# Kernel tuning notes

Hardware: AMD Instinct MI355X
Metric: run time of the kernel (lower is better)

## Reference

```python
import jax, jax.numpy as jnp
import numpy as np

A = -0.75  # torch bicubic coefficient
SCALES = [1.0, 0.9, 0.8, 0.7, 0.6]  # level=5
SOFTMAX_SCALE = 10.0
RES_SCALE = 1.0
ESCAPE_NAN = 1e-4


def _cubic_w(d):
    d = jnp.abs(d)
    return jnp.where(d <= 1.0, ((A + 2.0) * d - (A + 3.0)) * d * d + 1.0,
                     jnp.where(d < 2.0, ((A * d - 5.0 * A) * d + 8.0 * A) * d - 4.0 * A, 0.0))


def _resize_axis(x, out_size, axis):
    # bicubic, align_corners=True, 4-tap cubic conv with border clamp (matches torch)
    in_size = x.shape[axis]
    src = jnp.arange(out_size, dtype=jnp.float32) * (float(in_size - 1) / float(out_size - 1))
    i0 = jnp.floor(src).astype(jnp.int32)
    frac = src - i0.astype(jnp.float32)
    idx = jnp.clip(jnp.stack([i0 - 1, i0, i0 + 1, i0 + 2], 0), 0, in_size - 1)  # [4,out]
    w = jnp.stack([_cubic_w(frac + 1.0), _cubic_w(frac), _cubic_w(1.0 - frac), _cubic_w(2.0 - frac)], 0)  # [4,out]
    xm = jnp.moveaxis(x, axis, 0)
    g = xm[idx]  # [4,out,...]
    out = jnp.einsum('ko...,ko->o...', g, w)
    return jnp.moveaxis(out, 0, axis)


def bicubic_resize(x, oh, ow):
    return _resize_axis(_resize_axis(x, oh, 2), ow, 3)


def prelu(x, a):
    return jnp.where(x >= 0, x, a * x)


def conv1x1(x, W, b):
    # x [B,C,H,W], W [O,C], b [O]
    return jnp.einsum('oc,bchw->bohw', W, x) + b[None, :, None, None]


def extract_patches(x):
    # x [B,C,H,W] -> [B, H*W, C, 3, 3], 'same' padding, stride 1 (torch unfold order C,kh,kw)
    B, C, H, Wd = x.shape
    xp = jnp.pad(x, ((0, 0), (0, 0), (1, 1), (1, 1)))
    sl = [xp[:, :, dy:dy + H, dx:dx + Wd] for dy in range(3) for dx in range(3)]
    p = jnp.stack(sl, 0).reshape(3, 3, B, C, H, Wd)
    p = jnp.transpose(p, (2, 4, 5, 3, 0, 1))  # [B,H,W,C,3,3]
    return p.reshape(B, H * Wd, C, 3, 3)


def setup_inputs() -> dict:
    key = jax.random.key(0)
    ks = jax.random.split(key, 8)
    B, C, H, Wd = 2, 64, 64, 64
    Cm = 32
    return {
        'input': jax.random.normal(ks[0], (B, C, H, Wd), jnp.float32),
        'input_ref': jax.random.normal(ks[1], (B, C, H, Wd), jnp.float32),
        'Wb': jax.random.normal(ks[2], (Cm, C), jnp.float32) * 0.1,
        'bb': jax.random.normal(ks[3], (Cm,), jnp.float32) * 0.01,
        'Wm': jax.random.normal(ks[4], (Cm, C), jnp.float32) * 0.1,
        'bm': jax.random.normal(ks[5], (Cm,), jnp.float32) * 0.01,
        'Wa': jax.random.normal(ks[6], (C, C), jnp.float32) * 0.1,
        'ba': jax.random.normal(ks[7], (C,), jnp.float32) * 0.01,
        'a_prelu': jnp.full((1,), 0.25, jnp.float32),
    }


def reference(input, input_ref, Wb, bb, Wm, bm, Wa, ba, a_prelu):
    B, C, H, Wd = input.shape
    a = a_prelu[0]
    match_base = prelu(conv1x1(input, Wb, bb), a)  # [B,Cm,H,W]

    w_list, rw_list = [], []
    for s in SCALES:
        ref = input_ref if s == 1.0 else bicubic_resize(input_ref, int(H * s), int(Wd * s))
        base = prelu(conv1x1(ref, Wa, ba), a)   # conv_assembly
        rw_list.append(extract_patches(base))   # [B,Li,C,3,3]
        m = prelu(conv1x1(ref, Wm, bm), a)      # conv_match
        w_list.append(extract_patches(m))       # [B,Li,Cm,3,3]
    w = jnp.concatenate(w_list, axis=1)    # [B,L,Cm,3,3]
    rw = jnp.concatenate(rw_list, axis=1)  # [B,L,C,3,3]

    dn = ('NCHW', 'OIHW', 'NCHW')

    def per_sample(xi, wi, rwi):
        # xi [Cm,H,W]; wi [L,Cm,3,3]; rwi [L,C,3,3]
        nrm = jnp.maximum(jnp.sqrt(jnp.sum(wi * wi, axis=(1, 2, 3), keepdims=True)), ESCAPE_NAN)
        wn = wi / nrm
        scores = jax.lax.conv_general_dilated(xi[None], wn, (1, 1), [(1, 1), (1, 1)], dimension_numbers=dn)[0]  # [L,H,W]
        yi = jax.nn.softmax(scores * SOFTMAX_SCALE, axis=0)
        # conv_transpose2d(yi, rwi, stride=1, padding=1) == conv2d with flipped, transposed kernel, pad 1
        k = jnp.transpose(rwi, (1, 0, 2, 3))[:, :, ::-1, ::-1]  # [C,L,3,3]
        out = jax.lax.conv_general_dilated(yi[None], k, (1, 1), [(1, 1), (1, 1)], dimension_numbers=dn)[0] / 4.0
        return out  # [C,H,W]

    y = jax.vmap(per_sample)(match_base, w, rw)
    return y + input * RES_SCALE
```

## Files before the change

### kernel.cpp

```cpp
#include <hip/hip_runtime.h>
#include <stdint.h>


typedef __attribute__((ext_vector_type(8))) short bf16x8;
typedef __attribute__((ext_vector_type(4))) float f32x4;
typedef unsigned short ushort_t;

#define L_TOT  13326
#define NCHT   417
#define NPIX   4096
#define BCHUNK_E 9216
#define RCHUNK_E 18432
#define LOG2E10 14.4269504f
#define CT 256

__device__ __forceinline__ float cubw(float d) {
  d = fabsf(d);
  if (d <= 1.f) return (1.25f * d - 2.25f) * d * d + 1.f;
  if (d < 2.f)  return ((-0.75f * d + 3.75f) * d - 6.f) * d + 3.f;
  return 0.f;
}

__device__ __forceinline__ void decode_l(int l, int& S, int& off) {
  if (l < 4096)       { S = 64; off = 0; }
  else if (l < 7345)  { S = 57; off = 4096; }
  else if (l < 9946)  { S = 51; off = 7345; }
  else if (l < 11882) { S = 44; off = 9946; }
  else                { S = 38; off = 11882; }
}

__device__ __forceinline__ ushort_t f2bf(float f) {
  union { float f; uint32_t u; } v; v.f = f;
  uint32_t r = (v.u + 0x7fffu + ((v.u >> 16) & 1u)) >> 16;
  return (ushort_t)r;
}

__device__ __forceinline__ float preluf(float x, float a) { return x >= 0.f ? x : a * x; }

__device__ __forceinline__ void gll16(const ushort_t* g, ushort_t* l) {
  __builtin_amdgcn_global_load_lds(
      (const __attribute__((address_space(1))) unsigned int*)g,
      (__attribute__((address_space(3))) unsigned int*)l, 16, 0, 0);
}

__global__ void k_convref(const float* __restrict__ inref,
                          const float* __restrict__ Wm, const float* __restrict__ bm,
                          const float* __restrict__ Wa, const float* __restrict__ ba,
                          const float* __restrict__ ap,
                          float* __restrict__ mref, float* __restrict__ aref) {
  __shared__ float T[64][CT];
  __shared__ float Wy[CT][5], Wx[CT][5];
  __shared__ int   IY[CT], IX[CT];
  int blk = blockIdx.x;
  int oh = blk & 1; int lt = (blk >> 1) % 53; int b = blk / 106;
  int l0 = lt * CT;
  int tid = threadIdx.x;
  float a = ap[0];
  {
    int gl = l0 + tid;
    if (gl < L_TOT) {
      int S, off; decode_l(gl, S, off);
      int li = gl - off; int ly = li / S, lx = li % S;
      if (S == 64) {
        IY[tid] = -1; IX[tid] = ly * 64 + lx;
      } else {
        float sc = (float)(63.0 / (double)(S - 1));
        float sy = (float)ly * sc, sx = (float)lx * sc;
        int iy = (int)floorf(sy), ix = (int)floorf(sx);
        float fy = sy - (float)iy, fx = sx - (float)ix;
        IY[tid] = iy; IX[tid] = ix;
        Wy[tid][0] = cubw(fy + 1.f); Wy[tid][1] = cubw(fy);
        Wy[tid][2] = cubw(1.f - fy); Wy[tid][3] = cubw(2.f - fy);
        Wx[tid][0] = cubw(fx + 1.f); Wx[tid][1] = cubw(fx);
        Wx[tid][2] = cubw(1.f - fx); Wx[tid][3] = cubw(2.f - fx);
      }
    }
  }
  __syncthreads();
  for (int i = tid; i < 64 * CT; i += 256) {
    int c = i >> 8; int l2 = i & 255;
    int gl = l0 + l2;
    float val = 0.f;
    if (gl < L_TOT) {
      const float* img = inref + (size_t)(b * 64 + c) * 4096;
      int iy = IY[l2];
      if (iy == -1) {
        val = img[IX[l2]];
      } else {
        int ix = IX[l2];
        #pragma unroll
        for (int t = 0; t < 4; ++t) {
          int ty = iy - 1 + t; ty = ty < 0 ? 0 : (ty > 63 ? 63 : ty);
          float rv = 0.f;
          #pragma unroll
          for (int u = 0; u < 4; ++u) {
            int tx = ix - 1 + u; tx = tx < 0 ? 0 : (tx > 63 ? 63 : tx);
            rv += Wx[l2][u] * img[ty * 64 + tx];
          }
          val += Wy[l2][t] * rv;
        }
      }
    }
    T[c][l2] = val;
  }
  __syncthreads();
  int gl = l0 + tid;
  if (gl >= L_TOT) return;
  for (int oc = oh * 48; oc < oh * 48 + 48; ++oc) {
    const float* Wrow; float s;
    if (oc < 32) { Wrow = Wm + oc * 64; s = bm[oc]; }
    else         { Wrow = Wa + (oc - 32) * 64; s = ba[oc - 32]; }
    #pragma unroll 8
    for (int c = 0; c < 64; ++c) s += Wrow[c] * T[c][tid];
    s = preluf(s, a);
    if (oc < 32) mref[(size_t)(b * 32 + oc) * L_TOT + gl] = s;
    else         aref[(size_t)(b * 64 + oc - 32) * L_TOT + gl] = s;
  }
}

__global__ void k_mb(const float* __restrict__ input, const float* __restrict__ Wb,
                     const float* __restrict__ bb, const float* __restrict__ ap,
                     float* __restrict__ mbb, int n) {
  int idx = blockIdx.x * 256 + threadIdx.x;
  if (idx >= n) return;
  int p = idx % NPIX; int cm = (idx / NPIX) % 32; int b = idx / (32 * NPIX);
  float a = ap[0];
  float acc = bb[cm];
  for (int c = 0; c < 64; ++c) acc += Wb[cm * 64 + c] * input[(size_t)(b * 64 + c) * NPIX + p];
  mbb[(size_t)(b * 32 + cm) * NPIX + p] = preluf(acc, a);
}

__global__ void k_stage1(const float* __restrict__ mref, const float* __restrict__ mbb,
                         float* __restrict__ ssq, float* __restrict__ ssqA, int n) {
  int idx = blockIdx.x * 256 + threadIdx.x;
  if (idx >= n) return;
  if (idx < 2 * L_TOT) {
    int l = idx % L_TOT; int b = idx / L_TOT;
    float s = 0.f;
    for (int c = 0; c < 32; ++c) { float v = mref[(size_t)(b * 32 + c) * L_TOT + l]; s += v * v; }
    ssq[idx] = s;
  } else {
    int j = idx - 2 * L_TOT;
    int p = j % NPIX; int b = j / NPIX;
    float s = 0.f;
    for (int c = 0; c < 32; ++c) { float v = mbb[(size_t)(b * 32 + c) * NPIX + p]; s += v * v; }
    ssqA[j] = s;
  }
}

__global__ void k_stage2(const float* __restrict__ ssq, const float* __restrict__ ssqA,
                         float* __restrict__ invn, float* __restrict__ Mlog, int n) {
  int idx = blockIdx.x * 256 + threadIdx.x;
  if (idx >= n) return;
  if (idx < 2 * L_TOT) {
    int l = idx % L_TOT; int b = idx / L_TOT;
    int S, off; decode_l(l, S, off);
    int li = l - off; int ly = li / S, lx = li % S;
    float acc = 0.f;
    for (int dy = -1; dy <= 1; ++dy) {
      int ny = ly + dy; if (ny < 0 || ny >= S) continue;
      for (int dx = -1; dx <= 1; ++dx) {
        int nx = lx + dx; if (nx < 0 || nx >= S) continue;
        acc += ssq[(size_t)b * L_TOT + off + ny * S + nx];
      }
    }
    float nrm = sqrtf(acc); nrm = fmaxf(nrm, 1e-4f);
    invn[idx] = 1.f / nrm;
  } else {
    int j = idx - 2 * L_TOT;
    int p = j % NPIX; int b = j / NPIX;
    int y = p / 64, x = p % 64;
    float acc = 0.f;
    for (int dy = -1; dy <= 1; ++dy) {
      int ny = y + dy; if (ny < 0 || ny >= 64) continue;
      for (int dx = -1; dx <= 1; ++dx) {
        int nx = x + dx; if (nx < 0 || nx >= 64) continue;
        acc += ssqA[(size_t)b * NPIX + ny * 64 + nx];
      }
    }
    float qn = sqrtf(acc);
    float m = fmaxf(0.7f * qn, qn - 7.f);
    Mlog[j] = LOG2E10 * m;
  }
}

#define N_BS (2 * NCHT * 1152)
#define N_AIM (2 * NPIX * 36)
#define N_RS (2 * NCHT * 576 * 4)
__global__ void k_pack(const float* __restrict__ mref, const float* __restrict__ invn,
                       const float* __restrict__ mbb, const float* __restrict__ aref,
                       ushort_t* __restrict__ Bs, ushort_t* __restrict__ Am,
                       ushort_t* __restrict__ Rs, int n) {
  int idx = blockIdx.x * 256 + threadIdx.x;
  if (idx >= n) return;
  ushort_t v[8];
  if (idx < N_BS) {
    int segp = idx % 36; int col = (idx / 36) % 32;
    int ch = (idx / 1152) % NCHT; int b = idx / (1152 * NCHT);
    int segl = (segp & ~3) | ((segp & 3) ^ ((col >> 1) & 3));
    int l = ch * 32 + col;
    if (l < L_TOT) {
      int S, off; decode_l(l, S, off);
      int li = l - off; int ly = li / S, lx = li % S;
      float iv = invn[(size_t)b * L_TOT + l];
      #pragma unroll
      for (int e = 0; e < 8; ++e) {
        int k = segl * 8 + e;
        int c = k / 9; int r = k % 9; int dy = r / 3 - 1, dx = r % 3 - 1;
        int ny = ly + dy, nx = lx + dx;
        float val = 0.f;
        if (ny >= 0 && ny < S && nx >= 0 && nx < S)
          val = mref[(size_t)(b * 32 + c) * L_TOT + off + ny * S + nx] * iv;
        v[e] = f2bf(val);
      }
    } else {
      #pragma unroll
      for (int e = 0; e < 8; ++e) v[e] = 0;
    }
    *(uint4*)(Bs + ((size_t)(b * NCHT + ch) * BCHUNK_E + col * 288 + segp * 8)) = *(const uint4*)v;
  } else if (idx < N_BS + N_AIM) {
    int j = idx - N_BS;
    int k8 = j % 36; int p = (j / 36) % NPIX; int b = j / (36 * NPIX);
    int y = p / 64, x = p % 64;
    #pragma unroll
    for (int e = 0; e < 8; ++e) {
      int k = k8 * 8 + e;
      int c = k / 9; int r = k % 9; int dy = r / 3 - 1, dx = r % 3 - 1;
      int ny = y + dy, nx = x + dx;
      float val = 0.f;
      if (ny >= 0 && ny < 64 && nx >= 0 && nx < 64)
        val = mbb[(size_t)(b * 32 + c) * NPIX + ny * 64 + nx];
      v[e] = f2bf(val);
    }
    *(uint4*)(Am + ((size_t)(b * NPIX + p) * 288 + k8 * 8)) = *(const uint4*)v;
  } else {
    int j = idx - N_BS - N_AIM;
    int phys = j & 3; int q = j >> 2;
    int col = q % 576; q /= 576;
    int ch = q % NCHT; int b = q / NCHT;
    int c = col / 9; int r = col % 9; int dy = r / 3 - 1, dx = r % 3 - 1;
    int seg = phys ^ ((col >> 1) & 3);
    int lbase = ch * 32 + seg * 8;
    #pragma unroll
    for (int e = 0; e < 8; ++e) {
      int l = lbase + e;
      float val = 0.f;
      if (l < L_TOT) {
        int S, off; decode_l(l, S, off);
        int li = l - off; int ly = li / S, lx = li % S;
        int ny = ly + dy, nx = lx + dx;
        if (ny >= 0 && ny < S && nx >= 0 && nx < S)
          val = aref[(size_t)(b * 64 + c) * L_TOT + off + ny * S + nx];
      }
      v[e] = f2bf(val);
    }
    *(uint4*)(Rs + ((size_t)(b * NCHT + ch) * RCHUNK_E + col * 32 + phys * 8)) = *(const uint4*)v;
  }
}

__global__ __launch_bounds__(512, 2) void k_attn64(const ushort_t* __restrict__ Am,
                                                   const ushort_t* __restrict__ Bs,
                                                   const ushort_t* __restrict__ Rs,
                                                   const float* __restrict__ Mlog,
                                                   float* __restrict__ Og,
                                                   float* __restrict__ Ol) {
  __shared__ ushort_t Rl[3][RCHUNK_E];
  __shared__ ushort_t Bl[2][BCHUNK_E];
  __shared__ ushort_t Pl[2][2048];
  int tid = threadIdx.x;
  int xcd = blockIdx.x & 7; int slot = blockIdx.x >> 3;
  int group = xcd >> 1;
  int spl = group & 1; int b = group >> 1;
  int tile = slot * 2 + (xcd & 1);
  int p0 = tile * 64;
  int wave = tid >> 6, lane = tid & 63, quad = lane >> 4, ln = lane & 15;
  int rbS = wave & 3, cbh = wave >> 2;
  int g = wave & 3, zrh = wave >> 2;
  int c0 = spl ? 209 : 0, c1 = spl ? NCHT : 209;

  bf16x8 af[9];
  {
    const ushort_t* arow = Am + (size_t)(b * NPIX + p0 + rbS * 16 + ln) * 288;
    #pragma unroll
    for (int kk = 0; kk < 9; ++kk) af[kk] = *(const bf16x8*)(arow + kk * 32 + quad * 8);
  }
  float mlg[4];
  #pragma unroll
  for (int r = 0; r < 4; ++r)
    mlg[r] = Mlog[(size_t)b * NPIX + p0 + rbS * 16 + quad * 4 + r];

  f32x4 acc[2][9];
  #pragma unroll
  for (int h = 0; h < 2; ++h)
    #pragma unroll
    for (int t = 0; t < 9; ++t) { acc[h][t][0] = acc[h][t][1] = acc[h][t][2] = acc[h][t][3] = 0.f; }
  float psum[4] = {0.f, 0.f, 0.f, 0.f};

  const ushort_t* RsB = Rs + (size_t)b * NCHT * RCHUNK_E + lane * 8;
  const ushort_t* BsB = Bs + (size_t)b * NCHT * BCHUNK_E + lane * 8;

  {
    const ushort_t* sB0 = BsB + (size_t)c0 * BCHUNK_E;
    ushort_t* dB0 = Bl[c0 & 1];
    #pragma unroll
    for (int u = wave; u < 18; u += 8) gll16(sB0 + u * 512, dB0 + u * 512);
    const ushort_t* sB1 = BsB + (size_t)(c0 + 1) * BCHUNK_E;
    ushort_t* dB1 = Bl[(c0 + 1) & 1];
    #pragma unroll
    for (int u = wave; u < 18; u += 8) gll16(sB1 + u * 512, dB1 + u * 512);
    const ushort_t* sR = RsB + (size_t)c0 * RCHUNK_E;
    ushort_t* dR = Rl[c0 % 3];
    #pragma unroll
    for (int u = wave; u < 36; u += 8) gll16(sR + u * 512, dR + u * 512);
  }
  __syncthreads();

  int col32 = cbh * 16 + ln;
  int bswz = (col32 >> 1) & 3;
  int rpar = c0 % 3;
  for (int ch = c0; ch < c1; ++ch) {
    int par = ch & 1;
    int rnext = rpar == 2 ? 0 : rpar + 1;
    f32x4 sa, sb;
    sa[0] = sa[1] = sa[2] = sa[3] = 0.f;
    sb[0] = sb[1] = sb[2] = sb[3] = 0.f;
    #pragma unroll
    for (int kk = 0; kk < 9; ++kk) {
      int segp = kk * 4 + (quad ^ bswz);
      bf16x8 bf = *(const bf16x8*)&Bl[par][col32 * 288 + segp * 8];
      if (kk == 4 || kk == 5 || kk == 6 || kk == 7)
        sb = __builtin_amdgcn_mfma_f32_16x16x32_bf16(af[kk], bf, sb, 0, 0, 0);
      else
        sa = __builtin_amdgcn_mfma_f32_16x16x32_bf16(af[kk], bf, sa, 0, 0, 0);
    }
    int colw = ch * 32 + col32;
    bool valid = colw < L_TOT;
    #pragma unroll
    for (int r = 0; r < 4; ++r) {
      float sv = sa[r] + sb[r];
      float pv = valid ? exp2f(fmaf(sv, LOG2E10, -mlg[r])) : 0.f;
      int row = rbS * 16 + quad * 4 + r;
      int seg = cbh * 2 + (ln >> 3);
      int swz = seg ^ ((row >> 1) & 3);
      Pl[par][row * 32 + swz * 8 + (ln & 7)] = f2bf(pv);
      psum[r] += pv;
    }
    __syncthreads();
    if (ch + 2 < c1) {
      const ushort_t* sB = BsB + (size_t)(ch + 2) * BCHUNK_E;
      ushort_t* dB = Bl[par];
      #pragma unroll
      for (int u = wave; u < 18; u += 8) gll16(sB + u * 512, dB + u * 512);
    }
    if (ch + 1 < c1) {
      const ushort_t* sR = RsB + (size_t)(ch + 1) * RCHUNK_E;
      ushort_t* dR = Rl[rnext];
      #pragma unroll
      for (int u = wave; u < 36; u += 8) gll16(sR + u * 512, dR + u * 512);
    }
    bf16x8 pf0, pf1;
    {
      int sw = quad ^ ((ln >> 1) & 3);
      pf0 = *(const bf16x8*)&Pl[par][(zrh * 32 + ln) * 32 + sw * 8];
      pf1 = *(const bf16x8*)&Pl[par][(zrh * 32 + 16 + ln) * 32 + sw * 8];
    }
    #pragma unroll
    for (int t = 0; t < 9; ++t) {
      int col = g * 144 + t * 16 + ln;
      int swz = quad ^ ((col >> 1) & 3);
      bf16x8 rf = *(const bf16x8*)&Rl[rpar][col * 32 + swz * 8];
      acc[0][t] = __builtin_amdgcn_mfma_f32_16x16x32_bf16(pf0, rf, acc[0][t], 0, 0, 0);
      acc[1][t] = __builtin_amdgcn_mfma_f32_16x16x32_bf16(pf1, rf, acc[1][t], 0, 0, 0);
    }
    rpar = rnext;
  }

  #pragma unroll
  for (int m = 1; m <= 8; m <<= 1)
    #pragma unroll
    for (int r = 0; r < 4; ++r) psum[r] += __shfl_xor(psum[r], m);
  int sb2 = spl * 2 + b;
  if (ln == 0) {
    #pragma unroll
    for (int r = 0; r < 4; ++r) {
      int row = p0 + rbS * 16 + quad * 4 + r;
      Ol[(size_t)(sb2 * 2 + cbh) * NPIX + row] = psum[r];
    }
  }
  #pragma unroll
  for (int h = 0; h < 2; ++h)
    #pragma unroll
    for (int t = 0; t < 9; ++t) {
      int colg = g * 144 + t * 16 + ln;
      #pragma unroll
      for (int r = 0; r < 4; ++r) {
        int row = p0 + zrh * 32 + h * 16 + quad * 4 + r;
        Og[((size_t)sb2 * NPIX + row) * 576 + colg] = acc[h][t][r];
      }
    }
}

__global__ __launch_bounds__(512, 2) void k_attn128(const ushort_t* __restrict__ Am,
                                                    const ushort_t* __restrict__ Bs,
                                                    const ushort_t* __restrict__ Rs,
                                                    const float* __restrict__ Mlog,
                                                    float* __restrict__ Og,
                                                    float* __restrict__ Ol) {
  __shared__ ushort_t Rl[2][RCHUNK_E];
  __shared__ ushort_t Bl[2][BCHUNK_E];
  __shared__ ushort_t Pl[2][4096];
  int tid = threadIdx.x;
  int xcd = blockIdx.x & 7; int slot = blockIdx.x >> 3;
  int spl = xcd >> 1; int b = xcd & 1;
  int p0 = slot * 128;
  int wave = tid >> 6, lane = tid & 63, quad = lane >> 4, ln = lane & 15;
  int rb = wave;
  int g = wave & 3, zrh = wave >> 2;
  int c0 = (spl * NCHT) >> 2;
  int c1 = ((spl + 1) * NCHT) >> 2;

  bf16x8 af[9];
  {
    const ushort_t* arow = Am + (size_t)(b * NPIX + p0 + rb * 16 + ln) * 288;
    #pragma unroll
    for (int kk = 0; kk < 9; ++kk) af[kk] = *(const bf16x8*)(arow + kk * 32 + quad * 8);
  }
  float mlg[4], psum[4];
  #pragma unroll
  for (int r = 0; r < 4; ++r) {
    mlg[r] = Mlog[(size_t)b * NPIX + p0 + rb * 16 + quad * 4 + r];
    psum[r] = 0.f;
  }
  f32x4 acc[4][9];
  #pragma unroll
  for (int j = 0; j < 4; ++j)
    #pragma unroll
    for (int t = 0; t < 9; ++t) { acc[j][t][0] = acc[j][t][1] = acc[j][t][2] = acc[j][t][3] = 0.f; }

  const ushort_t* RsB = Rs + (size_t)b * NCHT * RCHUNK_E + lane * 8;
  const ushort_t* BsB = Bs + (size_t)b * NCHT * BCHUNK_E + lane * 8;

  auto stageB = [&](int chunk, int sl) {
    const ushort_t* s = BsB + (size_t)chunk * BCHUNK_E;
    ushort_t* d = Bl[sl];
    #pragma unroll
    for (int u = wave; u < 18; u += 8) gll16(s + u * 512, d + u * 512);
  };
  auto stageR = [&](int chunk, int sl) {
    const ushort_t* s = RsB + (size_t)chunk * RCHUNK_E;
    ushort_t* d = Rl[sl];
    #pragma unroll
    for (int u = wave; u < 36; u += 8) gll16(s + u * 512, d + u * 512);
  };

  int bswz = (ln >> 1) & 3;
  int psw = quad ^ ((ln >> 1) & 3);

  stageB(c0, 0);
  stageB(c0 + 1, 1);
  stageR(c0, 0);
  __syncthreads();

  for (int ch = c0; ch < c1; ++ch) {
    int par = ch & 1;
    f32x4 sA0, sB0, sA1, sB1;
    sA0[0]=sA0[1]=sA0[2]=sA0[3]=0.f; sB0[0]=sB0[1]=sB0[2]=sB0[3]=0.f;
    sA1[0]=sA1[1]=sA1[2]=sA1[3]=0.f; sB1[0]=sB1[1]=sB1[2]=sB1[3]=0.f;
    #pragma unroll
    for (int kk = 0; kk < 9; ++kk) {
      int segp = kk * 4 + (quad ^ bswz);
      bf16x8 bf0 = *(const bf16x8*)&Bl[par][(ln) * 288 + segp * 8];
      bf16x8 bf1 = *(const bf16x8*)&Bl[par][(16 + ln) * 288 + segp * 8];
      if (kk >= 4 && kk <= 7) {
        sB0 = __builtin_amdgcn_mfma_f32_16x16x32_bf16(af[kk], bf0, sB0, 0, 0, 0);
        sB1 = __builtin_amdgcn_mfma_f32_16x16x32_bf16(af[kk], bf1, sB1, 0, 0, 0);
      } else {
        sA0 = __builtin_amdgcn_mfma_f32_16x16x32_bf16(af[kk], bf0, sA0, 0, 0, 0);
        sA1 = __builtin_amdgcn_mfma_f32_16x16x32_bf16(af[kk], bf1, sA1, 0, 0, 0);
      }
    }
    bool valid0 = ch * 32 + ln < L_TOT;
    bool valid1 = ch * 32 + 16 + ln < L_TOT;
    #pragma unroll
    for (int r = 0; r < 4; ++r) {
      int row = rb * 16 + quad * 4 + r;
      int rsw = (row >> 1) & 3;
      float sv0 = sA0[r] + sB0[r];
      float pv0 = valid0 ? exp2f(fmaf(sv0, LOG2E10, -mlg[r])) : 0.f;
      int seg0 = 0 * 2 + (ln >> 3);
      Pl[par][row * 32 + (seg0 ^ rsw) * 8 + (ln & 7)] = f2bf(pv0);
      float sv1 = sA1[r] + sB1[r];
      float pv1 = valid1 ? exp2f(fmaf(sv1, LOG2E10, -mlg[r])) : 0.f;
      int seg1 = 1 * 2 + (ln >> 3);
      Pl[par][row * 32 + (seg1 ^ rsw) * 8 + (ln & 7)] = f2bf(pv1);
      psum[r] += pv0 + pv1;
    }
    __syncthreads();
    if (ch + 2 < c1) stageB(ch + 2, par);
    if (ch + 1 < c1) stageR(ch + 1, par ^ 1);
    bf16x8 pf[4];
    #pragma unroll
    for (int j = 0; j < 4; ++j)
      pf[j] = *(const bf16x8*)&Pl[par][(zrh * 64 + j * 16 + ln) * 32 + psw * 8];
    #pragma unroll
    for (int t = 0; t < 9; ++t) {
      int col = g * 144 + t * 16 + ln;
      int swz = quad ^ ((col >> 1) & 3);
      bf16x8 rf = *(const bf16x8*)&Rl[par][col * 32 + swz * 8];
      #pragma unroll
      for (int j = 0; j < 4; ++j)
        acc[j][t] = __builtin_amdgcn_mfma_f32_16x16x32_bf16(pf[j], rf, acc[j][t], 0, 0, 0);
    }
  }

  #pragma unroll
  for (int m = 1; m <= 8; m <<= 1)
    #pragma unroll
    for (int r = 0; r < 4; ++r) psum[r] += __shfl_xor(psum[r], m);
  int sb2 = spl * 2 + b;
  if (ln == 0) {
    #pragma unroll
    for (int r = 0; r < 4; ++r) {
      int row = p0 + rb * 16 + quad * 4 + r;
      Ol[(size_t)sb2 * NPIX + row] = psum[r];
    }
  }
  #pragma unroll
  for (int j = 0; j < 4; ++j)
    #pragma unroll
    for (int t = 0; t < 9; ++t) {
      int colg = g * 144 + t * 16 + ln;
      #pragma unroll
      for (int r = 0; r < 4; ++r) {
        int row = p0 + zrh * 64 + j * 16 + quad * 4 + r;
        Og[((size_t)sb2 * NPIX + row) * 576 + colg] = acc[j][t][r];
      }
    }
}

__global__ void k_inv(const float* __restrict__ Ol, float* __restrict__ inv, int n, int is128) {
  int idx = blockIdx.x * 256 + threadIdx.x;
  if (idx >= n) return;
  int b = idx / NPIX; int p = idx % NPIX;
  float s = 0.f;
  if (is128) {
    #pragma unroll
    for (int spl = 0; spl < 4; ++spl)
      s += Ol[(size_t)(spl * 2 + b) * NPIX + p];
  } else {
    #pragma unroll
    for (int spl = 0; spl < 2; ++spl)
      #pragma unroll
      for (int cbh = 0; cbh < 2; ++cbh)
        s += Ol[(size_t)(((spl * 2 + b) * 2) + cbh) * NPIX + p];
  }
  inv[idx] = 1.f / s;
}

template <int NSL>
__global__ void k_final(const float* __restrict__ Og, const float* __restrict__ inv,
                        const float* __restrict__ input, float* __restrict__ out) {
  __shared__ float T[16][65];
  int blk = blockIdx.x;
  int xq = blk & 3; int y = (blk >> 2) & 63; int b = blk >> 8;
  int tid = threadIdx.x;
  const size_t S1 = (size_t)2 * NPIX * 576;
  for (int it = 0; it < 4; ++it) {
    int lin = it * 256 + tid;
    int c = lin & 63, x16 = lin >> 6;
    int x = xq * 16 + x16;
    float acc = 0.f;
    #pragma unroll
    for (int j = 0; j < 3; ++j) {
      int qy = y + 1 - j; if (qy < 0 || qy >= 64) continue;
      #pragma unroll
      for (int i2 = 0; i2 < 3; ++i2) {
        int qx = x + 1 - i2; if (qx < 0 || qx >= 64) continue;
        int p = qy * 64 + qx;
        size_t e = ((size_t)b * NPIX + p) * 576 + c * 9 + j * 3 + i2;
        float tap = 0.f;
        #pragma unroll
        for (int s = 0; s < NSL; ++s) tap += Og[e + (size_t)s * S1];
        acc += tap * inv[b * NPIX + p];
      }
    }
    T[x16][c] = acc;
  }
  __syncthreads();
  for (int it = 0; it < 4; ++it) {
    int lin = it * 256 + tid;
    int x16 = lin & 15, c = lin >> 4;
    int o = ((b * 64 + c) * 64 + y) * 64 + xq * 16 + x16;
    out[o] = 0.25f * T[x16][c] + input[o];
  }
}

extern "C" void kernel_launch(void* const* d_in, const int* in_sizes, int n_in,
                              void* d_out, int out_size, void* d_ws, size_t ws_size,
                              hipStream_t stream) {
  (void)in_sizes; (void)n_in; (void)out_size;
  const float* input = (const float*)d_in[0];
  const float* inref = (const float*)d_in[1];
  const float* Wb = (const float*)d_in[2];
  const float* bb = (const float*)d_in[3];
  const float* Wm = (const float*)d_in[4];
  const float* bm = (const float*)d_in[5];
  const float* Wa = (const float*)d_in[6];
  const float* ba = (const float*)d_in[7];
  const float* ap = (const float*)d_in[8];
  float* out = (float*)d_out;

  char* ws = (char*)d_ws;
  size_t off = 0;
  auto alloc = [&](size_t bytes) -> char* {
    char* p = ws + off; off = (off + bytes + 255) & ~(size_t)255; return p;
  };
  ushort_t* Am   = (ushort_t*)alloc((size_t)2 * NPIX * 288 * 2);
  ushort_t* Bs   = (ushort_t*)alloc((size_t)2 * NCHT * BCHUNK_E * 2);
  ushort_t* Rs   = (ushort_t*)alloc((size_t)2 * NCHT * RCHUNK_E * 2);
  float*    Ol   = (float*)alloc((size_t)16 * NPIX * 4);
  float*    inv  = (float*)alloc((size_t)2 * NPIX * 4);
  float*    Mlog = (float*)alloc((size_t)2 * NPIX * 4);
  float*    ssqA = (float*)alloc((size_t)2 * NPIX * 4);
  size_t og64  = (size_t)4 * NPIX * 576 * 4;
  size_t og128 = og64 * 2;
  bool use128 = (off + og128 + 512) <= ws_size;
  char* big = alloc(use128 ? og128 : og64);
  float* Og = (float*)big;
  size_t eoff = 0;
  auto ealloc = [&](size_t bytes) -> char* {
    char* p = big + eoff; eoff = (eoff + bytes + 255) & ~(size_t)255; return p;
  };
  float* mref = (float*)ealloc((size_t)2 * 32 * L_TOT * 4);
  float* aref = (float*)ealloc((size_t)2 * 64 * L_TOT * 4);
  float* mbb  = (float*)ealloc((size_t)2 * 32 * NPIX * 4);
  float* ssq  = (float*)ealloc((size_t)2 * L_TOT * 4);
  float* invn = (float*)ealloc((size_t)2 * L_TOT * 4);

  k_convref<<<212, 256, 0, stream>>>(inref, Wm, bm, Wa, ba, ap, mref, aref);
  int n3 = 2 * 32 * NPIX;
  k_mb<<<(n3 + 255) / 256, 256, 0, stream>>>(input, Wb, bb, ap, mbb, n3);
  int ns = 2 * L_TOT + 2 * NPIX;
  k_stage1<<<(ns + 255) / 256, 256, 0, stream>>>(mref, mbb, ssq, ssqA, ns);
  k_stage2<<<(ns + 255) / 256, 256, 0, stream>>>(ssq, ssqA, invn, Mlog, ns);
  int np = N_BS + N_AIM + N_RS;
  k_pack<<<(np + 255) / 256, 256, 0, stream>>>(mref, invn, mbb, aref, Bs, Am, Rs, np);

  if (use128) {
    k_attn128<<<256, 512, 0, stream>>>(Am, Bs, Rs, Mlog, Og, Ol);
    k_inv<<<(2 * NPIX + 255) / 256, 256, 0, stream>>>(Ol, inv, 2 * NPIX, 1);
    k_final<4><<<512, 256, 0, stream>>>(Og, inv, input, out);
  } else {
    k_attn64<<<256, 512, 0, stream>>>(Am, Bs, Rs, Mlog, Og, Ol);
    k_inv<<<(2 * NPIX + 255) / 256, 256, 0, stream>>>(Ol, inv, 2 * NPIX, 0);
    k_final<2><<<512, 256, 0, stream>>>(Og, inv, input, out);
  }
}
```

Measured before the change: 449.0 us.

## Split attn128 work across 16 waves per block instead of 8

The 128-row attention kernel now launches 1024 threads per block. Each wave computes one 16-column half of the score tile and accumulates only 32 output rows instead of 64, which halves the accumulator registers per wave. Row sums are now written per column half, and k_inv is templated to sum both halves. This raises the number of waves that can hide latency, at the cost of duplicated A-fragment loads and more waves contending for the same LDS tiles and barriers.

```diff
diff --git a/kernel.cpp b/kernel.cpp
--- a/kernel.cpp
+++ b/kernel.cpp
@@ -400,12 +400,12 @@
     }
 }
 
-__global__ __launch_bounds__(512, 2) void k_attn128(const ushort_t* __restrict__ Am,
-                                                    const ushort_t* __restrict__ Bs,
-                                                    const ushort_t* __restrict__ Rs,
-                                                    const float* __restrict__ Mlog,
-                                                    float* __restrict__ Og,
-                                                    float* __restrict__ Ol) {
+__global__ __launch_bounds__(1024, 1) void k_attn128(const ushort_t* __restrict__ Am,
+                                                     const ushort_t* __restrict__ Bs,
+                                                     const ushort_t* __restrict__ Rs,
+                                                     const float* __restrict__ Mlog,
+                                                     float* __restrict__ Og,
+                                                     float* __restrict__ Ol) {
   __shared__ ushort_t Rl[2][RCHUNK_E];
   __shared__ ushort_t Bl[2][BCHUNK_E];
   __shared__ ushort_t Pl[2][4096];
@@ -414,8 +414,8 @@
   int spl = xcd >> 1; int b = xcd & 1;
   int p0 = slot * 128;
   int wave = tid >> 6, lane = tid & 63, quad = lane >> 4, ln = lane & 15;
-  int rb = wave;
-  int g = wave & 3, zrh = wave >> 2;
+  int rb = wave & 7, cbh = wave >> 3;
+  int g = wave & 3, zq = wave >> 2;
   int c0 = (spl * NCHT) >> 2;
   int c1 = ((spl + 1) * NCHT) >> 2;
 
@@ -431,9 +431,9 @@
     mlg[r] = Mlog[(size_t)b * NPIX + p0 + rb * 16 + quad * 4 + r];
     psum[r] = 0.f;
   }
-  f32x4 acc[4][9];
-  #pragma unroll
-  for (int j = 0; j < 4; ++j)
+  f32x4 acc[2][9];
+  #pragma unroll
+  for (int j = 0; j < 2; ++j)
     #pragma unroll
     for (int t = 0; t < 9; ++t) { acc[j][t][0] = acc[j][t][1] = acc[j][t][2] = acc[j][t][3] = 0.f; }
 
@@ -443,16 +443,15 @@
   auto stageB = [&](int chunk, int sl) {
     const ushort_t* s = BsB + (size_t)chunk * BCHUNK_E;
     ushort_t* d = Bl[sl];
-    #pragma unroll
-    for (int u = wave; u < 18; u += 8) gll16(s + u * 512, d + u * 512);
+    for (int u = wave; u < 18; u += 16) gll16(s + u * 512, d + u * 512);
   };
   auto stageR = [&](int chunk, int sl) {
     const ushort_t* s = RsB + (size_t)chunk * RCHUNK_E;
     ushort_t* d = Rl[sl];
-    #pragma unroll
-    for (int u = wave; u < 36; u += 8) gll16(s + u * 512, d + u * 512);
+    for (int u = wave; u < 36; u += 16) gll16(s + u * 512, d + u * 512);
   };
 
+  int col32 = cbh * 16 + ln;
   int bswz = (ln >> 1) & 3;
   int psw = quad ^ ((ln >> 1) & 3);
 
@@ -463,52 +462,43 @@
 
   for (int ch = c0; ch < c1; ++ch) {
     int par = ch & 1;
-    f32x4 sA0, sB0, sA1, sB1;
-    sA0[0]=sA0[1]=sA0[2]=sA0[3]=0.f; sB0[0]=sB0[1]=sB0[2]=sB0[3]=0.f;
-    sA1[0]=sA1[1]=sA1[2]=sA1[3]=0.f; sB1[0]=sB1[1]=sB1[2]=sB1[3]=0.f;
+    f32x4 sa, sb;
+    sa[0] = sa[1] = sa[2] = sa[3] = 0.f;
+    sb[0] = sb[1] = sb[2] = sb[3] = 0.f;
     #pragma unroll
     for (int kk = 0; kk < 9; ++kk) {
       int segp = kk * 4 + (quad ^ bswz);
-      bf16x8 bf0 = *(const bf16x8*)&Bl[par][(ln) * 288 + segp * 8];
-      bf16x8 bf1 = *(const bf16x8*)&Bl[par][(16 + ln) * 288 + segp * 8];
-      if (kk >= 4 && kk <= 7) {
-        sB0 = __builtin_amdgcn_mfma_f32_16x16x32_bf16(af[kk], bf0, sB0, 0, 0, 0);
-        sB1 = __builtin_amdgcn_mfma_f32_16x16x32_bf16(af[kk], bf1, sB1, 0, 0, 0);
-      } else {
-        sA0 = __builtin_amdgcn_mfma_f32_16x16x32_bf16(af[kk], bf0, sA0, 0, 0, 0);
-        sA1 = __builtin_amdgcn_mfma_f32_16x16x32_bf16(af[kk], bf1, sA1, 0, 0, 0);
-      }
-    }
-    bool valid0 = ch * 32 + ln < L_TOT;
-    bool valid1 = ch * 32 + 16 + ln < L_TOT;
+      bf16x8 bfrag = *(const bf16x8*)&Bl[par][col32 * 288 + segp * 8];
+      if (kk >= 4 && kk <= 7)
+        sb = __builtin_amdgcn_mfma_f32_16x16x32_bf16(af[kk], bfrag, sb, 0, 0, 0);
+      else
+        sa = __builtin_amdgcn_mfma_f32_16x16x32_bf16(af[kk], bfrag, sa, 0, 0, 0);
+    }
+    bool valid = ch * 32 + col32 < L_TOT;
     #pragma unroll
     for (int r = 0; r < 4; ++r) {
+      float sv = sa[r] + sb[r];
+      float pv = valid ? exp2f(fmaf(sv, LOG2E10, -mlg[r])) : 0.f;
       int row = rb * 16 + quad * 4 + r;
-      int rsw = (row >> 1) & 3;
-      float sv0 = sA0[r] + sB0[r];
-      float pv0 = valid0 ? exp2f(fmaf(sv0, LOG2E10, -mlg[r])) : 0.f;
-      int seg0 = 0 * 2 + (ln >> 3);
-      Pl[par][row * 32 + (seg0 ^ rsw) * 8 + (ln & 7)] = f2bf(pv0);
-      float sv1 = sA1[r] + sB1[r];
-      float pv1 = valid1 ? exp2f(fmaf(sv1, LOG2E10, -mlg[r])) : 0.f;
-      int seg1 = 1 * 2 + (ln >> 3);
-      Pl[par][row * 32 + (seg1 ^ rsw) * 8 + (ln & 7)] = f2bf(pv1);
-      psum[r] += pv0 + pv1;
+      int seg = cbh * 2 + (ln >> 3);
+      int swz = seg ^ ((row >> 1) & 3);
+      Pl[par][row * 32 + swz * 8 + (ln & 7)] = f2bf(pv);
+      psum[r] += pv;
     }
     __syncthreads();
     if (ch + 2 < c1) stageB(ch + 2, par);
     if (ch + 1 < c1) stageR(ch + 1, par ^ 1);
-    bf16x8 pf[4];
-    #pragma unroll
-    for (int j = 0; j < 4; ++j)
-      pf[j] = *(const bf16x8*)&Pl[par][(zrh * 64 + j * 16 + ln) * 32 + psw * 8];
+    bf16x8 pf[2];
+    #pragma unroll
+    for (int j = 0; j < 2; ++j)
+      pf[j] = *(const bf16x8*)&Pl[par][(zq * 32 + j * 16 + ln) * 32 + psw * 8];
     #pragma unroll
     for (int t = 0; t < 9; ++t) {
       int col = g * 144 + t * 16 + ln;
       int swz = quad ^ ((col >> 1) & 3);
       bf16x8 rf = *(const bf16x8*)&Rl[par][col * 32 + swz * 8];
       #pragma unroll
-      for (int j = 0; j < 4; ++j)
+      for (int j = 0; j < 2; ++j)
         acc[j][t] = __builtin_amdgcn_mfma_f32_16x16x32_bf16(pf[j], rf, acc[j][t], 0, 0, 0);
     }
   }
@@ -522,38 +512,33 @@
     #pragma unroll
     for (int r = 0; r < 4; ++r) {
       int row = p0 + rb * 16 + quad * 4 + r;
-      Ol[(size_t)sb2 * NPIX + row] = psum[r];
-    }
-  }
-  #pragma unroll
-  for (int j = 0; j < 4; ++j)
+      Ol[(size_t)(sb2 * 2 + cbh) * NPIX + row] = psum[r];
+    }
+  }
+  #pragma unroll
+  for (int j = 0; j < 2; ++j)
     #pragma unroll
     for (int t = 0; t < 9; ++t) {
       int colg = g * 144 + t * 16 + ln;
       #pragma unroll
       for (int r = 0; r < 4; ++r) {
-        int row = p0 + zrh * 64 + j * 16 + quad * 4 + r;
+        int row = p0 + zq * 32 + j * 16 + quad * 4 + r;
         Og[((size_t)sb2 * NPIX + row) * 576 + colg] = acc[j][t][r];
       }
     }
 }
 
-__global__ void k_inv(const float* __restrict__ Ol, float* __restrict__ inv, int n, int is128) {
+template <int NSPL>
+__global__ void k_inv(const float* __restrict__ Ol, float* __restrict__ inv, int n) {
   int idx = blockIdx.x * 256 + threadIdx.x;
   if (idx >= n) return;
   int b = idx / NPIX; int p = idx % NPIX;
   float s = 0.f;
-  if (is128) {
-    #pragma unroll
-    for (int spl = 0; spl < 4; ++spl)
-      s += Ol[(size_t)(spl * 2 + b) * NPIX + p];
-  } else {
-    #pragma unroll
-    for (int spl = 0; spl < 2; ++spl)
-      #pragma unroll
-      for (int cbh = 0; cbh < 2; ++cbh)
-        s += Ol[(size_t)(((spl * 2 + b) * 2) + cbh) * NPIX + p];
-  }
+  #pragma unroll
+  for (int spl = 0; spl < NSPL; ++spl)
+    #pragma unroll
+    for (int cbh = 0; cbh < 2; ++cbh)
+      s += Ol[(size_t)(((spl * 2 + b) * 2) + cbh) * NPIX + p];
   inv[idx] = 1.f / s;
 }
 
@@ -647,12 +632,12 @@
   k_pack<<<(np + 255) / 256, 256, 0, stream>>>(mref, invn, mbb, aref, Bs, Am, Rs, np);
 
   if (use128) {
-    k_attn128<<<256, 512, 0, stream>>>(Am, Bs, Rs, Mlog, Og, Ol);
-    k_inv<<<(2 * NPIX + 255) / 256, 256, 0, stream>>>(Ol, inv, 2 * NPIX, 1);
+    k_attn128<<<256, 1024, 0, stream>>>(Am, Bs, Rs, Mlog, Og, Ol);
+    k_inv<4><<<(2 * NPIX + 255) / 256, 256, 0, stream>>>(Ol, inv, 2 * NPIX);
     k_final<4><<<512, 256, 0, stream>>>(Og, inv, input, out);
   } else {
     k_attn64<<<256, 512, 0, stream>>>(Am, Bs, Rs, Mlog, Og, Ol);
-    k_inv<<<(2 * NPIX + 255) / 256, 256, 0, stream>>>(Ol, inv, 2 * NPIX, 0);
+    k_inv<2><<<(2 * NPIX + 255) / 256, 256, 0, stream>>>(Ol, inv, 2 * NPIX);
     k_final<2><<<512, 256, 0, stream>>>(Og, inv, input, out);
   }
 }
```

Result: slower. 734.3 us (+63.5%).

## Stage Og rows in shared memory with float4 loads in final fold kernel

Applied to the files above, without the earlier changes.

The final col2im-style fold kernel now handles half an image row per block. For each of the three source rows it cooperatively loads 34 neighbouring pixels' 576-wide Og vectors into shared memory using float4 loads, with the split-sum and inverse normalisation applied during the load. Each thread then accumulates 8 channels from shared memory. This replaces scattered strided scalar gathers with coalesced vector reads, at the cost of about 78 KB of LDS per block and half as many blocks. k_inv is also templated on its mode flag.

```diff
diff --git a/kernel.cpp b/kernel.cpp
--- a/kernel.cpp
+++ b/kernel.cpp
@@ -538,12 +538,13 @@
     }
 }
 
-__global__ void k_inv(const float* __restrict__ Ol, float* __restrict__ inv, int n, int is128) {
+template <int IS128>
+__global__ void k_inv(const float* __restrict__ Ol, float* __restrict__ inv, int n) {
   int idx = blockIdx.x * 256 + threadIdx.x;
   if (idx >= n) return;
   int b = idx / NPIX; int p = idx % NPIX;
   float s = 0.f;
-  if (is128) {
+  if (IS128) {
     #pragma unroll
     for (int spl = 0; spl < 4; ++spl)
       s += Ol[(size_t)(spl * 2 + b) * NPIX + p];
@@ -558,40 +559,59 @@
 }
 
 template <int NSL>
-__global__ void k_final(const float* __restrict__ Og, const float* __restrict__ inv,
-                        const float* __restrict__ input, float* __restrict__ out) {
-  __shared__ float T[16][65];
+__global__ __launch_bounds__(256) void k_final(const float* __restrict__ Og,
+                                               const float* __restrict__ inv,
+                                               const float* __restrict__ input,
+                                               float* __restrict__ out) {
+  __shared__ float Srow[34][577];
   int blk = blockIdx.x;
-  int xq = blk & 3; int y = (blk >> 2) & 63; int b = blk >> 8;
+  int xh = blk & 1; int y = (blk >> 1) & 63; int b = blk >> 7;
   int tid = threadIdx.x;
   const size_t S1 = (size_t)2 * NPIX * 576;
-  for (int it = 0; it < 4; ++it) {
-    int lin = it * 256 + tid;
-    int c = lin & 63, x16 = lin >> 6;
-    int x = xq * 16 + x16;
-    float acc = 0.f;
-    #pragma unroll
-    for (int j = 0; j < 3; ++j) {
-      int qy = y + 1 - j; if (qy < 0 || qy >= 64) continue;
-      #pragma unroll
-      for (int i2 = 0; i2 < 3; ++i2) {
-        int qx = x + 1 - i2; if (qx < 0 || qx >= 64) continue;
+  int x32 = tid & 31, c0 = (tid >> 5) * 8;
+  int qx0 = xh * 32 - 1;
+  float acc[8];
+  #pragma unroll
+  for (int i = 0; i < 8; ++i) acc[i] = 0.f;
+
+  for (int j = 0; j < 3; ++j) {
+    int qy = y + 1 - j;
+    if (qy < 0 || qy >= 64) continue;
+    for (int u = tid; u < 34 * 144; u += 256) {
+      int k = u / 144; int f4 = u - k * 144;
+      int qx = qx0 + k;
+      float vx = 0.f, vy = 0.f, vz = 0.f, vw = 0.f;
+      if (qx >= 0 && qx < 64) {
         int p = qy * 64 + qx;
-        size_t e = ((size_t)b * NPIX + p) * 576 + c * 9 + j * 3 + i2;
-        float tap = 0.f;
+        size_t e = ((size_t)b * NPIX + p) * 576 + f4 * 4;
+        float iv = inv[b * NPIX + p];
         #pragma unroll
-        for (int s = 0; s < NSL; ++s) tap += Og[e + (size_t)s * S1];
-        acc += tap * inv[b * NPIX + p];
-      }
-    }
-    T[x16][c] = acc;
-  }
-  __syncthreads();
-  for (int it = 0; it < 4; ++it) {
-    int lin = it * 256 + tid;
-    int x16 = lin & 15, c = lin >> 4;
-    int o = ((b * 64 + c) * 64 + y) * 64 + xq * 16 + x16;
-    out[o] = 0.25f * T[x16][c] + input[o];
+        for (int s = 0; s < NSL; ++s) {
+          const float4 t4 = *(const float4*)(Og + e + (size_t)s * S1);
+          vx += t4.x; vy += t4.y; vz += t4.z; vw += t4.w;
+        }
+        vx *= iv; vy *= iv; vz *= iv; vw *= iv;
+      }
+      float* d = &Srow[k][f4 * 4];
+      d[0] = vx; d[1] = vy; d[2] = vz; d[3] = vw;
+    }
+    __syncthreads();
+    #pragma unroll
+    for (int i2 = 0; i2 < 3; ++i2) {
+      int k = x32 + 2 - i2;
+      #pragma unroll
+      for (int cc = 0; cc < 8; ++cc)
+        acc[cc] += Srow[k][(c0 + cc) * 9 + j * 3 + i2];
+    }
+    __syncthreads();
+  }
+
+  int x = xh * 32 + x32;
+  #pragma unroll
+  for (int cc = 0; cc < 8; ++cc) {
+    int c = c0 + cc;
+    int o = ((b * 64 + c) * 64 + y) * 64 + x;
+    out[o] = 0.25f * acc[cc] + input[o];
   }
 }
 
@@ -648,11 +668,11 @@
 
   if (use128) {
     k_attn128<<<256, 512, 0, stream>>>(Am, Bs, Rs, Mlog, Og, Ol);
-    k_inv<<<(2 * NPIX + 255) / 256, 256, 0, stream>>>(Ol, inv, 2 * NPIX, 1);
-    k_final<4><<<512, 256, 0, stream>>>(Og, inv, input, out);
+    k_inv<1><<<(2 * NPIX + 255) / 256, 256, 0, stream>>>(Ol, inv, 2 * NPIX);
+    k_final<4><<<256, 256, 0, stream>>>(Og, inv, input, out);
   } else {
     k_attn64<<<256, 512, 0, stream>>>(Am, Bs, Rs, Mlog, Og, Ol);
-    k_inv<<<(2 * NPIX + 255) / 256, 256, 0, stream>>>(Ol, inv, 2 * NPIX, 0);
-    k_final<2><<<512, 256, 0, stream>>>(Og, inv, input, out);
-  }
-}
+    k_inv<0><<<(2 * NPIX + 255) / 256, 256, 0, stream>>>(Ol, inv, 2 * NPIX);
+    k_final<2><<<256, 256, 0, stream>>>(Og, inv, input, out);
+  }
+}
```

After: 439.0 us. 1.02x faster.
